# Optimization experiments

Hardware: AMD Instinct MI355X
Metric: run time of the kernel (lower is better)

The kernel has to match this reference:

```python
import jax, jax.numpy as jnp
import numpy as np

K = 16          # top-k per pooled row
EPS = 1e-12     # tf.nn.l2_normalize epsilon


def setup_inputs() -> dict:
    key = jax.random.key(0)
    x = jax.random.normal(key, (16, 256, 128, 128), dtype=jnp.float32)
    return {"x": x}


def reference(x) -> tuple:
    # x: [B, C, H, W]; last_n_dims = 2 -> pool the trailing H*W axis.
    B, C, H, W = x.shape
    flat = x.reshape(B, C, H * W)                       # [B, C, HW]
    # tf.nn.l2_normalize(axis=-1): x / sqrt(max(sum(x^2), eps))
    sq = jnp.sum(flat * flat, axis=-1, keepdims=True)
    normed = flat * jax.lax.rsqrt(jnp.maximum(sq, EPS))  # [B, C, HW]
    top_k_value, top_k_idx = jax.lax.top_k(normed, K)    # [B, C, K]
    # decode flat indices into (h, w) coordinates (div/mod loop in original)
    h = top_k_idx // W
    w = top_k_idx % W
    coors = jnp.stack([h, w], axis=-1).astype(jnp.int32)  # [B, C, K, 2]
    return top_k_value, coors
```

## Files before the change

### kernel.cpp

```cpp
#include <hip/hip_runtime.h>


#define KSEL 16
#define HW   16384
#define WDIM 128
#define CAP  1024
#define T0   2.5f
#define NROWS 4096
#define NT   512
#define PER  8
#define VALS_TOTAL (NROWS * KSEL)

__global__ __launch_bounds__(NT, 8) void topk_rows(const float* __restrict__ x,
                                                   float* __restrict__ out) {
    const int row  = blockIdx.x;
    const int t    = threadIdx.x;
    const int lane = t & 63;

    __shared__ unsigned long long s_cand[CAP];
    __shared__ unsigned s_cnt;
    __shared__ float s_part[NT / 64];
    __shared__ float s_scale;

    const float4* rowp = (const float4*)(x + (size_t)row * HW);

    float4 buf[PER];
    #pragma unroll
    for (int k = 0; k < PER; ++k) buf[k] = rowp[k * NT + t];

    float sumsq = 0.0f;
    #pragma unroll
    for (int k = 0; k < PER; ++k) {
        sumsq = fmaf(buf[k].x, buf[k].x, sumsq);
        sumsq = fmaf(buf[k].y, buf[k].y, sumsq);
        sumsq = fmaf(buf[k].z, buf[k].z, sumsq);
        sumsq = fmaf(buf[k].w, buf[k].w, sumsq);
    }
    #pragma unroll
    for (int off = 32; off > 0; off >>= 1)
        sumsq += __shfl_down(sumsq, off, 64);
    if (lane == 0) s_part[t >> 6] = sumsq;
    __syncthreads();
    if (t == 0) {
        float tot = 0.0f;
        #pragma unroll
        for (int i = 0; i < NT / 64; ++i) tot += s_part[i];
        s_scale = 1.0f / sqrtf(fmaxf(tot, 1e-12f));
    }

    float T = T0, lo = -3.0e38f, hi = 3.0e38f;
    unsigned cnt = 0;
    for (int attempt = 0; attempt < 25; ++attempt) {
        __syncthreads();
        if (t == 0) s_cnt = 0;
        __syncthreads();

        unsigned msk = 0;
        #pragma unroll
        for (int k = 0; k < PER; ++k) {
            msk |= (buf[k].x > T) ? (1u << (4 * k + 0)) : 0u;
            msk |= (buf[k].y > T) ? (1u << (4 * k + 1)) : 0u;
            msk |= (buf[k].z > T) ? (1u << (4 * k + 2)) : 0u;
            msk |= (buf[k].w > T) ? (1u << (4 * k + 3)) : 0u;
        }
        unsigned base = 0;
        if (msk) base = atomicAdd(&s_cnt, (unsigned)__popc(msk));
        if (msk) {
            #pragma unroll
            for (int k = 0; k < PER; ++k) {
                #pragma unroll
                for (int c = 0; c < 4; ++c) {
                    float v = (c == 0) ? buf[k].x : (c == 1) ? buf[k].y
                            : (c == 2) ? buf[k].z : buf[k].w;
                    if (v > T) {
                        if (base < CAP) {
                            unsigned u  = __float_as_uint(v);
                            unsigned mm = u ^ (((unsigned)((int)u >> 31)) | 0x80000000u);
                            int idx = (k * NT + t) * 4 + c;
                            s_cand[base] = ((unsigned long long)mm << 32) |
                                           (unsigned)(16383 - idx);
                        }
                        base++;
                    }
                }
            }
        }
        __syncthreads();
        cnt = s_cnt;
        if (cnt >= KSEL && cnt <= CAP) break;
        if (cnt < KSEL) { hi = T; T = (lo < -1.0e38f) ? T - 1.0f : 0.5f * (lo + T); }
        else            { lo = T; T = (hi >  1.0e38f) ? T + 1.0f : 0.5f * (T + hi); }
    }
    if (cnt > CAP) cnt = CAP;
    const float scale = s_scale;

    for (unsigned i = t; i < cnt; i += NT) {
        unsigned long long p = s_cand[i];
        unsigned m = (unsigned)(p >> 32);
        unsigned u = (m & 0x80000000u) ? (m ^ 0x80000000u) : ~m;
        float vn = __uint_as_float(u) * scale;
        unsigned u2 = __float_as_uint(vn);
        unsigned m2 = u2 ^ (((unsigned)((int)u2 >> 31)) | 0x80000000u);
        s_cand[i] = ((unsigned long long)m2 << 32) | (p & 0xFFFFFFFFull);
    }
    __syncthreads();

    for (unsigned i = t; i < cnt; i += NT) {
        unsigned long long p = s_cand[i];
        int rank = 0;
        for (unsigned j = 0; j < cnt; ++j) rank += (s_cand[j] > p) ? 1 : 0;
        if (rank < KSEL) {
            unsigned m = (unsigned)(p >> 32);
            unsigned u = (m & 0x80000000u) ? (m ^ 0x80000000u) : ~m;
            float vn = __uint_as_float(u);
            int idx = 16383 - (int)(unsigned)(p & 0xFFFFFFFFull);
            out[row * KSEL + rank] = vn;
            float* coor = out + VALS_TOTAL + ((size_t)row * KSEL + rank) * 2;
            coor[0] = (float)(idx >> 7);
            coor[1] = (float)(idx & (WDIM - 1));
        }
    }
}

extern "C" void kernel_launch(void* const* d_in, const int* in_sizes, int n_in,
                              void* d_out, int out_size, void* d_ws, size_t ws_size,
                              hipStream_t stream) {
    const float* x = (const float*)d_in[0];
    float* out = (float*)d_out;
    topk_rows<<<NROWS, NT, 0, stream>>>(x, out);
}
```

Baseline: 391.2 us.

## Halve block size, use nontemporal loads, and peel first threshold pass

Changes the block to 256 threads each holding 16 float4 values (64 elements per thread), drops the occupancy hint in launch_bounds, and loads the row with nontemporal vector loads. The first threshold pass is peeled out of the search loop so the common case skips two barriers and the loop bookkeeping. The intent is to cut per-row barrier overhead and cache pollution from streaming input. The cost is higher register pressure per thread, which may reduce occupancy, and a 64-bit candidate mask.

Result: faster. 355.2 us (-9.2%).

```diff
diff --git a/kernel.cpp b/kernel.cpp
--- a/kernel.cpp
+++ b/kernel.cpp
@@ -7,12 +7,14 @@
 #define CAP  1024
 #define T0   2.5f
 #define NROWS 4096
-#define NT   512
-#define PER  8
+#define NT   256
+#define PER  16
 #define VALS_TOTAL (NROWS * KSEL)
 
-__global__ __launch_bounds__(NT, 8) void topk_rows(const float* __restrict__ x,
-                                                   float* __restrict__ out) {
+typedef float floatx4 __attribute__((ext_vector_type(4)));
+
+__global__ __launch_bounds__(NT) void topk_rows(const float* __restrict__ x,
+                                                float* __restrict__ out) {
     const int row  = blockIdx.x;
     const int t    = threadIdx.x;
     const int lane = t & 63;
@@ -22,11 +24,12 @@
     __shared__ float s_part[NT / 64];
     __shared__ float s_scale;
 
-    const float4* rowp = (const float4*)(x + (size_t)row * HW);
+    const floatx4* rowp = (const floatx4*)(x + (size_t)row * HW);
 
-    float4 buf[PER];
+    floatx4 buf[PER];
     #pragma unroll
-    for (int k = 0; k < PER; ++k) buf[k] = rowp[k * NT + t];
+    for (int k = 0; k < PER; ++k)
+        buf[k] = __builtin_nontemporal_load(&rowp[k * NT + t]);
 
     float sumsq = 0.0f;
     #pragma unroll
@@ -40,6 +43,7 @@
     for (int off = 32; off > 0; off >>= 1)
         sumsq += __shfl_down(sumsq, off, 64);
     if (lane == 0) s_part[t >> 6] = sumsq;
+    if (t == 0) s_cnt = 0;
     __syncthreads();
     if (t == 0) {
         float tot = 0.0f;
@@ -48,50 +52,83 @@
         s_scale = 1.0f / sqrtf(fmaxf(tot, 1e-12f));
     }
 
-    float T = T0, lo = -3.0e38f, hi = 3.0e38f;
-    unsigned cnt = 0;
-    for (int attempt = 0; attempt < 25; ++attempt) {
-        __syncthreads();
-        if (t == 0) s_cnt = 0;
-        __syncthreads();
-
-        unsigned msk = 0;
+    float T = T0;
+    unsigned long long msk = 0;
+    #pragma unroll
+    for (int k = 0; k < PER; ++k) {
+        msk |= (buf[k].x > T) ? (1ull << (4 * k + 0)) : 0ull;
+        msk |= (buf[k].y > T) ? (1ull << (4 * k + 1)) : 0ull;
+        msk |= (buf[k].z > T) ? (1ull << (4 * k + 2)) : 0ull;
+        msk |= (buf[k].w > T) ? (1ull << (4 * k + 3)) : 0ull;
+    }
+    unsigned base = 0;
+    if (msk) base = atomicAdd(&s_cnt, (unsigned)__popcll(msk));
+    if (msk) {
         #pragma unroll
         for (int k = 0; k < PER; ++k) {
-            msk |= (buf[k].x > T) ? (1u << (4 * k + 0)) : 0u;
-            msk |= (buf[k].y > T) ? (1u << (4 * k + 1)) : 0u;
-            msk |= (buf[k].z > T) ? (1u << (4 * k + 2)) : 0u;
-            msk |= (buf[k].w > T) ? (1u << (4 * k + 3)) : 0u;
+            #pragma unroll
+            for (int c = 0; c < 4; ++c) {
+                float v = (c == 0) ? buf[k].x : (c == 1) ? buf[k].y
+                        : (c == 2) ? buf[k].z : buf[k].w;
+                if (v > T) {
+                    if (base < CAP) {
+                        unsigned u  = __float_as_uint(v);
+                        unsigned mm = u ^ (((unsigned)((int)u >> 31)) | 0x80000000u);
+                        int idx = (k * NT + t) * 4 + c;
+                        s_cand[base] = ((unsigned long long)mm << 32) |
+                                       (unsigned)(16383 - idx);
+                    }
+                    base++;
+                }
+            }
         }
-        unsigned base = 0;
-        if (msk) base = atomicAdd(&s_cnt, (unsigned)__popc(msk));
-        if (msk) {
+    }
+    __syncthreads();
+    unsigned cnt = s_cnt;
+
+    if (cnt < KSEL || cnt > CAP) {
+        float lo = -3.0e38f, hi = 3.0e38f;
+        for (int attempt = 0; attempt < 24 && (cnt < KSEL || cnt > CAP); ++attempt) {
+            if (cnt < KSEL) { hi = T; T = (lo < -1.0e38f) ? T - 1.0f : 0.5f * (lo + T); }
+            else            { lo = T; T = (hi >  1.0e38f) ? T + 1.0f : 0.5f * (T + hi); }
+            __syncthreads();
+            if (t == 0) s_cnt = 0;
+            __syncthreads();
+            msk = 0;
             #pragma unroll
             for (int k = 0; k < PER; ++k) {
+                msk |= (buf[k].x > T) ? (1ull << (4 * k + 0)) : 0ull;
+                msk |= (buf[k].y > T) ? (1ull << (4 * k + 1)) : 0ull;
+                msk |= (buf[k].z > T) ? (1ull << (4 * k + 2)) : 0ull;
+                msk |= (buf[k].w > T) ? (1ull << (4 * k + 3)) : 0ull;
+            }
+            base = 0;
+            if (msk) base = atomicAdd(&s_cnt, (unsigned)__popcll(msk));
+            if (msk) {
                 #pragma unroll
-                for (int c = 0; c < 4; ++c) {
-                    float v = (c == 0) ? buf[k].x : (c == 1) ? buf[k].y
-                            : (c == 2) ? buf[k].z : buf[k].w;
-                    if (v > T) {
-                        if (base < CAP) {
-                            unsigned u  = __float_as_uint(v);
-                            unsigned mm = u ^ (((unsigned)((int)u >> 31)) | 0x80000000u);
-                            int idx = (k * NT + t) * 4 + c;
-                            s_cand[base] = ((unsigned long long)mm << 32) |
-                                           (unsigned)(16383 - idx);
+                for (int k = 0; k < PER; ++k) {
+                    #pragma unroll
+                    for (int c = 0; c < 4; ++c) {
+                        float v = (c == 0) ? buf[k].x : (c == 1) ? buf[k].y
+                                : (c == 2) ? buf[k].z : buf[k].w;
+                        if (v > T) {
+                            if (base < CAP) {
+                                unsigned u  = __float_as_uint(v);
+                                unsigned mm = u ^ (((unsigned)((int)u >> 31)) | 0x80000000u);
+                                int idx = (k * NT + t) * 4 + c;
+                                s_cand[base] = ((unsigned long long)mm << 32) |
+                                               (unsigned)(16383 - idx);
+                            }
+                            base++;
                         }
-                        base++;
                     }
                 }
             }
+            __syncthreads();
+            cnt = s_cnt;
         }
-        __syncthreads();
-        cnt = s_cnt;
-        if (cnt >= KSEL && cnt <= CAP) break;
-        if (cnt < KSEL) { hi = T; T = (lo < -1.0e38f) ? T - 1.0f : 0.5f * (lo + T); }
-        else            { lo = T; T = (hi >  1.0e38f) ? T + 1.0f : 0.5f * (T + hi); }
+        if (cnt > CAP) cnt = CAP;
     }
-    if (cnt > CAP) cnt = CAP;
     const float scale = s_scale;
 
     for (unsigned i = t; i < cnt; i += NT) {
```

## Split top-k into quarter-row streaming kernel and per-row candidate selection kernel

Applied to the files above, without the earlier changes.

The single per-row kernel becomes two. The first kernel launches four blocks per row, each streaming a quarter of the row with nontemporal loads; each block computes a partial sum of squares and collects candidates above a fixed threshold into workspace. The second kernel merges the partial sums and candidate lists per row, falling back to a global-memory threshold search if any quarter overflowed or too few candidates were found. This aims for more parallelism and fewer registers per thread during the bandwidth-bound pass, at the cost of an extra launch and a workspace round trip.

Result: faster. 337.8 us (-13.7%).

```diff
diff --git a/kernel.cpp b/kernel.cpp
--- a/kernel.cpp
+++ b/kernel.cpp
@@ -3,98 +3,165 @@
 
 #define KSEL 16
 #define HW   16384
+#define QSZ  4096
 #define WDIM 128
 #define CAP  1024
+#define CAPQ 256
 #define T0   2.5f
 #define NROWS 4096
-#define NT   512
-#define PER  8
+#define NQ   (NROWS * 4)
 #define VALS_TOTAL (NROWS * KSEL)
 
-__global__ __launch_bounds__(NT, 8) void topk_rows(const float* __restrict__ x,
-                                                   float* __restrict__ out) {
-    const int row  = blockIdx.x;
+typedef float floatx4 __attribute__((ext_vector_type(4)));
+
+
+__global__ __launch_bounds__(256) void k1_stream(const float* __restrict__ x,
+                                                 float* __restrict__ qsum,
+                                                 unsigned* __restrict__ qcnt,
+                                                 unsigned long long* __restrict__ qcand) {
+    const int b    = blockIdx.x;
+    const int row  = b >> 2;
+    const int q    = b & 3;
     const int t    = threadIdx.x;
     const int lane = t & 63;
 
-    __shared__ unsigned long long s_cand[CAP];
+    __shared__ unsigned long long s_cand[CAPQ];
     __shared__ unsigned s_cnt;
-    __shared__ float s_part[NT / 64];
-    __shared__ float s_scale;
-
-    const float4* rowp = (const float4*)(x + (size_t)row * HW);
-
-    float4 buf[PER];
-    #pragma unroll
-    for (int k = 0; k < PER; ++k) buf[k] = rowp[k * NT + t];
+    __shared__ float s_part[4];
+
+    if (t == 0) s_cnt = 0;
+    __syncthreads();
+
+    const floatx4* p = (const floatx4*)(x + (size_t)row * HW + q * QSZ);
+
+    floatx4 buf[4];
+    #pragma unroll
+    for (int k = 0; k < 4; ++k)
+        buf[k] = __builtin_nontemporal_load(&p[k * 256 + t]);
 
     float sumsq = 0.0f;
     #pragma unroll
-    for (int k = 0; k < PER; ++k) {
+    for (int k = 0; k < 4; ++k) {
         sumsq = fmaf(buf[k].x, buf[k].x, sumsq);
         sumsq = fmaf(buf[k].y, buf[k].y, sumsq);
         sumsq = fmaf(buf[k].z, buf[k].z, sumsq);
         sumsq = fmaf(buf[k].w, buf[k].w, sumsq);
     }
+
+    unsigned msk = 0;
+    #pragma unroll
+    for (int k = 0; k < 4; ++k) {
+        msk |= (buf[k].x > T0) ? (1u << (4 * k + 0)) : 0u;
+        msk |= (buf[k].y > T0) ? (1u << (4 * k + 1)) : 0u;
+        msk |= (buf[k].z > T0) ? (1u << (4 * k + 2)) : 0u;
+        msk |= (buf[k].w > T0) ? (1u << (4 * k + 3)) : 0u;
+    }
+    unsigned base = 0;
+    if (msk) base = atomicAdd(&s_cnt, (unsigned)__popc(msk));
+    if (msk) {
+        #pragma unroll
+        for (int k = 0; k < 4; ++k) {
+            #pragma unroll
+            for (int c = 0; c < 4; ++c) {
+                float v = (c == 0) ? buf[k].x : (c == 1) ? buf[k].y
+                        : (c == 2) ? buf[k].z : buf[k].w;
+                if (v > T0) {
+                    if (base < CAPQ) {
+                        unsigned u  = __float_as_uint(v);
+                        unsigned mm = u ^ (((unsigned)((int)u >> 31)) | 0x80000000u);
+                        int idx = q * QSZ + (k * 256 + t) * 4 + c;
+                        s_cand[base] = ((unsigned long long)mm << 32) |
+                                       (unsigned)(16383 - idx);
+                    }
+                    base++;
+                }
+            }
+        }
+    }
+
     #pragma unroll
     for (int off = 32; off > 0; off >>= 1)
         sumsq += __shfl_down(sumsq, off, 64);
     if (lane == 0) s_part[t >> 6] = sumsq;
     __syncthreads();
+
+    unsigned cnt = s_cnt;
+    unsigned wr = cnt < CAPQ ? cnt : CAPQ;
+    for (unsigned i = t; i < wr; i += 256)
+        qcand[(size_t)b * CAPQ + i] = s_cand[i];
     if (t == 0) {
-        float tot = 0.0f;
+        qcnt[b] = cnt;
+        qsum[b] = s_part[0] + s_part[1] + s_part[2] + s_part[3];
+    }
+}
+
+__global__ __launch_bounds__(256) void k2_select(const float* __restrict__ x,
+                                                 const float* __restrict__ qsum,
+                                                 const unsigned* __restrict__ qcnt,
+                                                 const unsigned long long* __restrict__ qcand,
+                                                 float* __restrict__ out) {
+    const int row = blockIdx.x;
+    const int t   = threadIdx.x;
+
+    __shared__ unsigned long long s_cand[CAP];
+    __shared__ unsigned s_qc[4];
+    __shared__ float s_qs[4];
+    __shared__ unsigned s_cnt;
+    __shared__ float s_scale;
+
+    if (t < 4) {
+        s_qc[t] = qcnt[row * 4 + t];
+        s_qs[t] = qsum[row * 4 + t];
+    }
+    __syncthreads();
+
+    const unsigned c0 = s_qc[0], c1 = s_qc[1], c2 = s_qc[2], c3 = s_qc[3];
+    if (t == 0)
+        s_scale = 1.0f / sqrtf(fmaxf(s_qs[0] + s_qs[1] + s_qs[2] + s_qs[3], 1e-12f));
+    const bool ovf = (c0 > CAPQ) | (c1 > CAPQ) | (c2 > CAPQ) | (c3 > CAPQ);
+    const unsigned tot = c0 + c1 + c2 + c3;
+
+    unsigned cnt;
+    if (!ovf && tot >= KSEL && tot <= CAP) {
+        const unsigned off[4] = {0u, c0, c0 + c1, c0 + c1 + c2};
+        const unsigned cc[4]  = {c0, c1, c2, c3};
         #pragma unroll
-        for (int i = 0; i < NT / 64; ++i) tot += s_part[i];
-        s_scale = 1.0f / sqrtf(fmaxf(tot, 1e-12f));
-    }
-
-    float T = T0, lo = -3.0e38f, hi = 3.0e38f;
-    unsigned cnt = 0;
-    for (int attempt = 0; attempt < 25; ++attempt) {
+        for (int q = 0; q < 4; ++q)
+            for (unsigned i = t; i < cc[q]; i += 256)
+                s_cand[off[q] + i] = qcand[(size_t)(row * 4 + q) * CAPQ + i];
+        cnt = tot;
         __syncthreads();
-        if (t == 0) s_cnt = 0;
-        __syncthreads();
-
-        unsigned msk = 0;
-        #pragma unroll
-        for (int k = 0; k < PER; ++k) {
-            msk |= (buf[k].x > T) ? (1u << (4 * k + 0)) : 0u;
-            msk |= (buf[k].y > T) ? (1u << (4 * k + 1)) : 0u;
-            msk |= (buf[k].z > T) ? (1u << (4 * k + 2)) : 0u;
-            msk |= (buf[k].w > T) ? (1u << (4 * k + 3)) : 0u;
-        }
-        unsigned base = 0;
-        if (msk) base = atomicAdd(&s_cnt, (unsigned)__popc(msk));
-        if (msk) {
-            #pragma unroll
-            for (int k = 0; k < PER; ++k) {
-                #pragma unroll
-                for (int c = 0; c < 4; ++c) {
-                    float v = (c == 0) ? buf[k].x : (c == 1) ? buf[k].y
-                            : (c == 2) ? buf[k].z : buf[k].w;
-                    if (v > T) {
-                        if (base < CAP) {
-                            unsigned u  = __float_as_uint(v);
-                            unsigned mm = u ^ (((unsigned)((int)u >> 31)) | 0x80000000u);
-                            int idx = (k * NT + t) * 4 + c;
-                            s_cand[base] = ((unsigned long long)mm << 32) |
-                                           (unsigned)(16383 - idx);
-                        }
-                        base++;
+    } else {
+        const float* xr = x + (size_t)row * HW;
+        float T = T0, lo = -3.0e38f, hi = 3.0e38f;
+        cnt = 0;
+        for (int it = 0; it < 32; ++it) {
+            __syncthreads();
+            if (t == 0) s_cnt = 0;
+            __syncthreads();
+            for (int i = t; i < HW; i += 256) {
+                float v = xr[i];
+                if (v > T) {
+                    unsigned slot = atomicAdd(&s_cnt, 1u);
+                    if (slot < CAP) {
+                        unsigned u  = __float_as_uint(v);
+                        unsigned mm = u ^ (((unsigned)((int)u >> 31)) | 0x80000000u);
+                        s_cand[slot] = ((unsigned long long)mm << 32) |
+                                       (unsigned)(16383 - i);
                     }
                 }
             }
+            __syncthreads();
+            cnt = s_cnt;
+            if (cnt >= KSEL && cnt <= CAP) break;
+            if (cnt < KSEL) { hi = T; T = (lo < -1.0e38f) ? T - 1.0f : 0.5f * (lo + T); }
+            else            { lo = T; T = (hi >  1.0e38f) ? T + 1.0f : 0.5f * (T + hi); }
         }
-        __syncthreads();
-        cnt = s_cnt;
-        if (cnt >= KSEL && cnt <= CAP) break;
-        if (cnt < KSEL) { hi = T; T = (lo < -1.0e38f) ? T - 1.0f : 0.5f * (lo + T); }
-        else            { lo = T; T = (hi >  1.0e38f) ? T + 1.0f : 0.5f * (T + hi); }
-    }
-    if (cnt > CAP) cnt = CAP;
+        if (cnt > CAP) cnt = CAP;
+    }
     const float scale = s_scale;
 
-    for (unsigned i = t; i < cnt; i += NT) {
+    for (unsigned i = t; i < cnt; i += 256) {
         unsigned long long p = s_cand[i];
         unsigned m = (unsigned)(p >> 32);
         unsigned u = (m & 0x80000000u) ? (m ^ 0x80000000u) : ~m;
@@ -105,7 +172,7 @@
     }
     __syncthreads();
 
-    for (unsigned i = t; i < cnt; i += NT) {
+    for (unsigned i = t; i < cnt; i += 256) {
         unsigned long long p = s_cand[i];
         int rank = 0;
         for (unsigned j = 0; j < cnt; ++j) rank += (s_cand[j] > p) ? 1 : 0;
@@ -127,5 +194,12 @@
                               hipStream_t stream) {
     const float* x = (const float*)d_in[0];
     float* out = (float*)d_out;
-    topk_rows<<<NROWS, NT, 0, stream>>>(x, out);
+    char* ws = (char*)d_ws;
+    float* qsum = (float*)ws;
+    unsigned* qcnt = (unsigned*)(ws + 64 * 1024);
+    unsigned long long* qcand =
+        (unsigned long long*)(ws + 128 * 1024);
+
+    k1_stream<<<NQ, 256, 0, stream>>>(x, qsum, qcnt, qcand);
+    k2_select<<<NROWS, 256, 0, stream>>>(x, qsum, qcnt, qcand, out);
 }
```
